# Performance work log

Hardware: AMD Instinct MI355X
Metric: run time of the kernel (lower is better)

Reference implementation:

```python
import jax, jax.numpy as jnp
import numpy as np

B, N, DIM, H, DH = 8, 1024, 768, 12, 64
INNER = H * DH
SCALE = DH ** -0.5


def _bias_idx(n):
    # Reproduce the offset->id mapping from the torch __init__ loop:
    # offsets are first seen in row-major (p1, p2) order, so
    # id(0)=0, id(-k)=k (k=1..n-1), id(+k)=n-1+k.
    i = np.arange(n)[:, None]
    j = np.arange(n)[None, :]
    off = i - j
    idx = np.where(off <= 0, -off, n - 1 + off)
    return jnp.asarray(idx, dtype=jnp.int32)  # (n, n), values in [0, 2n-2]


def setup_inputs() -> dict:
    key = jax.random.key(0)
    ks = jax.random.split(key, 5)
    x = jax.random.normal(ks[0], (B, N, DIM), dtype=jnp.float32)
    w_qkv = jax.random.normal(ks[1], (DIM, 3 * INNER), dtype=jnp.float32) * (DIM ** -0.5)
    bias_table = jax.random.normal(ks[2], (H, 2 * N - 1), dtype=jnp.float32) * 0.02
    w_out = jax.random.normal(ks[3], (INNER, DIM), dtype=jnp.float32) * (INNER ** -0.5)
    b_out = jnp.zeros((DIM,), dtype=jnp.float32)
    bias_idx = _bias_idx(N)
    return {"x": x, "w_qkv": w_qkv, "bias_table": bias_table,
            "w_out": w_out, "b_out": b_out, "bias_idx": bias_idx}


def reference(x, w_qkv, bias_table, w_out, b_out, bias_idx):
    b, n, _ = x.shape
    qkv = x @ w_qkv  # (b, n, 3*inner)
    q, k, v = jnp.split(qkv, 3, axis=-1)
    def heads(t):
        return t.reshape(b, n, H, DH).transpose(0, 2, 1, 3)  # (b, h, n, d)
    q, k, v = heads(q), heads(k), heads(v)
    bias = bias_table[:, bias_idx]  # (h, n, n), gathered per-head relpos bias
    dots = jnp.einsum('bhid,bhjd->bhij', q, k) * SCALE + bias[None]
    attn = jax.nn.softmax(dots, axis=-1)
    out = jnp.einsum('bhij,bhjd->bhid', attn, v)
    out = out.transpose(0, 2, 1, 3).reshape(b, n, INNER)
    return out @ w_out + b_out
```

## Files before the change

### kernel.cpp

```cpp
#include <hip/hip_runtime.h>
#include <hip/hip_bf16.h>
#include <stdint.h>

typedef unsigned short u16;
typedef unsigned int u32;
typedef __bf16 bf16x8 __attribute__((ext_vector_type(8)));
typedef float f32x4 __attribute__((ext_vector_type(4)));
typedef unsigned short u16x4 __attribute__((ext_vector_type(4)));
typedef unsigned int u32x2 __attribute__((ext_vector_type(2)));

#define SEQ     1024
#define DIM     768
#define NH      12
#define QKV_LD  2304
#define LOG2E   1.4426950408889634f
#define C1      0.18033688f

__device__ __forceinline__ u16 f2bf(float f) {
    union { float f; unsigned v; } x; x.f = f;
    unsigned r = (x.v + 0x7FFFu + ((x.v >> 16) & 1u)) >> 16;
    return (u16)r;
}
__device__ __forceinline__ void store_out(u16* p, float v)  { *p = f2bf(v); }
__device__ __forceinline__ void store_out(float* p, float v){ *p = v; }

__device__ __forceinline__ void async16(void* lds, const void* g) {
    __builtin_amdgcn_global_load_lds(
        (const __attribute__((address_space(1))) unsigned*)(uintptr_t)g,
        (__attribute__((address_space(3))) unsigned*)(unsigned)(uintptr_t)lds,
        16, 0, 0);
}

__device__ __forceinline__ int sw32(int row, int q) {
    return row * 32 + (q ^ ((row >> 1) & 3)) * 8;
}
__device__ __forceinline__ const bf16x8 ld64(const u16* base, int row, int cg) {
    return *(const bf16x8*)&base[row * 64 + (cg ^ (row & 7)) * 8];
}

__global__ __launch_bounds__(256) void cvt_k(const float* __restrict__ in,
                                             u16* __restrict__ out) {
    int i = (blockIdx.x * 256 + threadIdx.x) * 4;
    float4 v = *(const float4*)(in + i);
    u16x4 o = { f2bf(v.x), f2bf(v.y), f2bf(v.z), f2bf(v.w) };
    *(u16x4*)(out + i) = o;
}

__global__ __launch_bounds__(256) void transpose_k(const float* __restrict__ in,
                                                   u16* __restrict__ out,
                                                   int R, int C) {
    __shared__ __align__(16) float t[32][33];
    int c0 = blockIdx.x * 32, r0 = blockIdx.y * 32;
    int tx = threadIdx.x & 31, ty = threadIdx.x >> 5;
#pragma unroll
    for (int i = 0; i < 32; i += 8)
        t[ty + i][tx] = in[(size_t)(r0 + ty + i) * C + c0 + tx];
    __syncthreads();
#pragma unroll
    for (int i = 0; i < 32; i += 8)
        out[(size_t)(c0 + ty + i) * R + r0 + tx] = f2bf(t[tx][ty + i]);
}

__global__ __launch_bounds__(256) void vt_k(const u16* __restrict__ qkv,
                                            u16* __restrict__ vT) {
    __shared__ __align__(16) u16 t[32][33];
    int bh = blockIdx.z;
    int b = bh / 12, h = bh % 12;
    int key0 = blockIdx.x * 32, dh0 = blockIdx.y * 32;
    int tx = threadIdx.x & 31, ty = threadIdx.x >> 5;
#pragma unroll
    for (int i = 0; i < 32; i += 8)
        t[ty + i][tx] = qkv[(size_t)(b * SEQ + key0 + ty + i) * QKV_LD +
                            1536 + h * 64 + dh0 + tx];
    __syncthreads();
#pragma unroll
    for (int i = 0; i < 32; i += 8)
        vT[(size_t)(bh * 64 + dh0 + ty + i) * SEQ + key0 + tx] = t[tx][ty + i];
}

template <int HAS_BIAS, typename OUT_T>
__global__ __launch_bounds__(256) void gemm_bt(const u16* __restrict__ A,
                                               const u16* __restrict__ Bt,
                                               const float* __restrict__ bias,
                                               OUT_T* __restrict__ C,
                                               int M, int N, int K) {
    __shared__ __align__(16) u16 sA[128 * 32];
    __shared__ __align__(16) u16 sB[128 * 32];
    const int tid = threadIdx.x;
    const int lane = tid & 63;
    const int quad = lane >> 4, l16 = lane & 15;
    const int wave = tid >> 6;
    const int m0 = blockIdx.y * 128, n0 = blockIdx.x * 128;
    const int wm = (wave >> 1) * 64, wn = (wave & 1) * 64;

    f32x4 acc[4][4] = {};

    for (int k0 = 0; k0 < K; k0 += 32) {
        __syncthreads();
#pragma unroll
        for (int rep = 0; rep < 2; ++rep) {
            int i = rep * 256 + wave * 64 + lane;
            int row = i >> 2;
            int q = (i & 3) ^ ((row >> 1) & 3);
            async16(&sA[i * 8], A + (size_t)(m0 + row) * K + k0 + q * 8);
            async16(&sB[i * 8], Bt + (size_t)(n0 + row) * K + k0 + q * 8);
        }
        __syncthreads();

        bf16x8 af[4], bfr[4];
#pragma unroll
        for (int mi = 0; mi < 4; ++mi)
            af[mi] = *(const bf16x8*)&sA[sw32(wm + mi * 16 + l16, quad)];
#pragma unroll
        for (int nj = 0; nj < 4; ++nj)
            bfr[nj] = *(const bf16x8*)&sB[sw32(wn + nj * 16 + l16, quad)];
#pragma unroll
        for (int mi = 0; mi < 4; ++mi)
#pragma unroll
            for (int nj = 0; nj < 4; ++nj)
                acc[mi][nj] = __builtin_amdgcn_mfma_f32_16x16x32_bf16(
                    af[mi], bfr[nj], acc[mi][nj], 0, 0, 0);
    }

#pragma unroll
    for (int mi = 0; mi < 4; ++mi) {
#pragma unroll
        for (int nj = 0; nj < 4; ++nj) {
            int col = n0 + wn + nj * 16 + l16;
            float bv = HAS_BIAS ? bias[col] : 0.0f;
#pragma unroll
            for (int r = 0; r < 4; ++r) {
                int row = m0 + wm + mi * 16 + quad * 4 + r;
                store_out(&C[(size_t)row * N + col], acc[mi][nj][r] + bv);
            }
        }
    }
}

__global__ __launch_bounds__(256) void attn_k(const u16* __restrict__ qkv,
                                              const u16* __restrict__ vT,
                                              const float* __restrict__ bias_table,
                                              u16* __restrict__ out) {
    __shared__ __align__(16) u16 sK[64 * 64];
    __shared__ __align__(16) u16 sV[64 * 64];
    __shared__ __align__(16) float sBias[2048];
    __shared__ __align__(16) u16 sP[4][32 * 64];
    __shared__ __align__(16) float sLsum[4][32];

    const int tid = threadIdx.x;
    const int wave = tid >> 6, lane = tid & 63;
    const int quad = lane >> 4, l16 = lane & 15;
    const int h = blockIdx.y, b = blockIdx.z;
    const int q0 = blockIdx.x * 128, wq = wave * 32;

    for (int i = tid; i < 2047; i += 256)
        sBias[i] = LOG2E * bias_table[h * 2047 + (i <= 1023 ? 1023 - i : i)];

    bf16x8 qf[2][2];
#pragma unroll
    for (int nt = 0; nt < 2; ++nt)
#pragma unroll
        for (int hf = 0; hf < 2; ++hf)
            qf[nt][hf] = *(const bf16x8*)(qkv +
                (size_t)(b * SEQ + q0 + wq + nt * 16 + l16) * QKV_LD +
                h * 64 + hf * 32 + quad * 8);

    f32x4 o[2][4] = {};
    float lsum[2] = {0.f, 0.f};
    u16* sPw = sP[wave];

    for (int kt = 0; kt < SEQ / 64; ++kt) {
        __syncthreads();
#pragma unroll
        for (int rep = 0; rep < 2; ++rep) {
            int i = rep * 256 + wave * 64 + lane;
            int row = i >> 3;
            int c = (i & 7) ^ (row & 7);
            async16(&sK[i * 8],
                    qkv + (size_t)(b * SEQ + kt * 64 + row) * QKV_LD + 768 + h * 64 + c * 8);
            async16(&sV[i * 8],
                    vT + (size_t)((b * NH + h) * 64 + row) * SEQ + kt * 64 + c * 8);
        }
        __syncthreads();

#pragma unroll
        for (int mt = 0; mt < 4; ++mt) {
            int krow = mt * 16 + l16;
            bf16x8 af0 = ld64(sK, krow, quad);
            bf16x8 af1 = ld64(sK, krow, 4 + quad);
#pragma unroll
            for (int nt = 0; nt < 2; ++nt) {
                f32x4 s = {0.f, 0.f, 0.f, 0.f};
                s = __builtin_amdgcn_mfma_f32_16x16x32_bf16(af0, qf[nt][0], s, 0, 0, 0);
                s = __builtin_amdgcn_mfma_f32_16x16x32_bf16(af1, qf[nt][1], s, 0, 0, 0);
                int dbase = (q0 + wq + nt * 16 + l16) -
                            (kt * 64 + mt * 16 + quad * 4) + 1023;
                u32 u[4];
#pragma unroll
                for (int r = 0; r < 4; ++r) {
                    float arg = s[r] * C1 + sBias[dbase - r];
                    float p = exp2f(fminf(arg, 30.0f));
                    lsum[nt] += p;
                    u[r] = __float_as_uint(p) + 0x8000u;
                }
                u32x2 pk = { __builtin_amdgcn_perm(u[1], u[0], 0x07060302u),
                             __builtin_amdgcn_perm(u[3], u[2], 0x07060302u) };
                int qrow = nt * 16 + l16;
                int sc = (mt * 2 + (quad >> 1)) ^ (qrow & 7);
                *(u32x2*)&sPw[qrow * 64 + sc * 8 + (quad & 1) * 4] = pk;
            }
        }

        bf16x8 pf[2][2];
#pragma unroll
        for (int mtp = 0; mtp < 2; ++mtp) {
            int prow = mtp * 16 + l16;
            pf[mtp][0] = ld64(sPw, prow, quad);
            pf[mtp][1] = ld64(sPw, prow, 4 + quad);
        }
#pragma unroll
        for (int c4 = 0; c4 < 4; ++c4) {
            int vrow = c4 * 16 + l16;
            bf16x8 vf0 = ld64(sV, vrow, quad);
            bf16x8 vf1 = ld64(sV, vrow, 4 + quad);
#pragma unroll
            for (int mtp = 0; mtp < 2; ++mtp) {
                o[mtp][c4] = __builtin_amdgcn_mfma_f32_16x16x32_bf16(
                    pf[mtp][0], vf0, o[mtp][c4], 0, 0, 0);
                o[mtp][c4] = __builtin_amdgcn_mfma_f32_16x16x32_bf16(
                    pf[mtp][1], vf1, o[mtp][c4], 0, 0, 0);
            }
        }
    }

#pragma unroll
    for (int nt = 0; nt < 2; ++nt) {
        float s = lsum[nt];
        s += __shfl_xor(s, 16, 64);
        s += __shfl_xor(s, 32, 64);
        if (quad == 0) sLsum[wave][nt * 16 + l16] = s;
    }
#pragma unroll
    for (int mtp = 0; mtp < 2; ++mtp) {
        f32x4 ls = *(const f32x4*)&sLsum[wave][mtp * 16 + quad * 4];
#pragma unroll
        for (int c4 = 0; c4 < 4; ++c4)
#pragma unroll
            for (int r = 0; r < 4; ++r) {
                int qrow = q0 + wq + mtp * 16 + quad * 4 + r;
                out[(size_t)(b * SEQ + qrow) * DIM + h * 64 + c4 * 16 + l16] =
                    f2bf(o[mtp][c4][r] / ls[r]);
            }
    }
}

extern "C" void kernel_launch(void* const* d_in, const int* in_sizes, int n_in,
                              void* d_out, int out_size, void* d_ws, size_t ws_size,
                              hipStream_t stream) {
    const float* x          = (const float*)d_in[0];
    const float* w_qkv      = (const float*)d_in[1];
    const float* bias_table = (const float*)d_in[2];
    const float* w_out      = (const float*)d_in[3];
    const float* b_out      = (const float*)d_in[4];
    float* out = (float*)d_out;

    char* ws = (char*)d_ws;
    u16* ws_qkv   = (u16*)(ws);
    u16* ws_attn  = (u16*)(ws + 37748736);
    u16* ws_xb    = (u16*)(ws + 50331648);
    u16* ws_wqkvT = (u16*)(ws + 62914560);
    u16* ws_woutT = (u16*)(ws + 66453504);
    u16* ws_vT    = (u16*)(ws + 67633152);

    cvt_k<<<8 * 1024 * 768 / 1024, 256, 0, stream>>>(x, ws_xb);
    transpose_k<<<dim3(2304 / 32, 768 / 32), 256, 0, stream>>>(w_qkv, ws_wqkvT, 768, 2304);
    transpose_k<<<dim3(768 / 32, 768 / 32), 256, 0, stream>>>(w_out, ws_woutT, 768, 768);

    gemm_bt<0, u16><<<dim3(2304 / 128, 8192 / 128), 256, 0, stream>>>(
        ws_xb, ws_wqkvT, nullptr, ws_qkv, 8192, 2304, 768);

    vt_k<<<dim3(SEQ / 32, 2, 8 * NH), 256, 0, stream>>>(ws_qkv, ws_vT);

    attn_k<<<dim3(SEQ / 128, NH, 8), 256, 0, stream>>>(ws_qkv, ws_vT, bias_table, ws_attn);

    gemm_bt<1, float><<<dim3(768 / 128, 8192 / 128), 256, 0, stream>>>(
        ws_attn, ws_woutT, b_out, out, 8192, 768, 768);
}
```

Before: 230.6 us.

## Load K/V fragments directly from global memory and switch PV matmul to fp16

The attention kernel no longer stages K and V tiles in shared memory through async loads and two block-wide barriers per key tile. Each wave now reads its MFMA fragments straight from global memory and relies on the cache. V is stored transposed in fp16, P is packed to fp16 with cvt_pkrtz, and the PV product uses the f16 MFMA. The exp clamp is lowered to 15 so values stay within fp16 range. This drops the barriers and LDS traffic but makes each wave fetch the same K/V data separately, with uncoalesced strided global loads that may add latency.

New measurement: 263.1 us. 14.1% more time.

```diff
diff --git a/kernel.cpp b/kernel.cpp
--- a/kernel.cpp
+++ b/kernel.cpp
@@ -5,9 +5,11 @@
 typedef unsigned short u16;
 typedef unsigned int u32;
 typedef __bf16 bf16x8 __attribute__((ext_vector_type(8)));
+typedef _Float16 f16x8 __attribute__((ext_vector_type(8)));
+typedef _Float16 f16x2 __attribute__((ext_vector_type(2)));
+typedef __fp16 hf16x2 __attribute__((ext_vector_type(2)));
 typedef float f32x4 __attribute__((ext_vector_type(4)));
 typedef unsigned short u16x4 __attribute__((ext_vector_type(4)));
-typedef unsigned int u32x2 __attribute__((ext_vector_type(2)));
 
 #define SEQ     1024
 #define DIM     768
@@ -16,6 +18,9 @@
 #define LOG2E   1.4426950408889634f
 #define C1      0.18033688f
 
+__device__ __forceinline__ float bf2f(u16 u) {
+    union { unsigned v; float f; } x; x.v = ((unsigned)u) << 16; return x.f;
+}
 __device__ __forceinline__ u16 f2bf(float f) {
     union { float f; unsigned v; } x; x.f = f;
     unsigned r = (x.v + 0x7FFFu + ((x.v >> 16) & 1u)) >> 16;
@@ -33,9 +38,6 @@
 
 __device__ __forceinline__ int sw32(int row, int q) {
     return row * 32 + (q ^ ((row >> 1) & 3)) * 8;
-}
-__device__ __forceinline__ const bf16x8 ld64(const u16* base, int row, int cg) {
-    return *(const bf16x8*)&base[row * 64 + (cg ^ (row & 7)) * 8];
 }
 
 __global__ __launch_bounds__(256) void cvt_k(const float* __restrict__ in,
@@ -62,7 +64,7 @@
 }
 
 __global__ __launch_bounds__(256) void vt_k(const u16* __restrict__ qkv,
-                                            u16* __restrict__ vT) {
+                                            _Float16* __restrict__ vT) {
     __shared__ __align__(16) u16 t[32][33];
     int bh = blockIdx.z;
     int b = bh / 12, h = bh % 12;
@@ -75,7 +77,8 @@
     __syncthreads();
 #pragma unroll
     for (int i = 0; i < 32; i += 8)
-        vT[(size_t)(bh * 64 + dh0 + ty + i) * SEQ + key0 + tx] = t[tx][ty + i];
+        vT[(size_t)(bh * 64 + dh0 + ty + i) * SEQ + key0 + tx] =
+            (_Float16)bf2f(t[tx][ty + i]);
 }
 
 template <int HAS_BIAS, typename OUT_T>
@@ -138,13 +141,11 @@
 }
 
 __global__ __launch_bounds__(256) void attn_k(const u16* __restrict__ qkv,
-                                              const u16* __restrict__ vT,
+                                              const _Float16* __restrict__ vT,
                                               const float* __restrict__ bias_table,
                                               u16* __restrict__ out) {
-    __shared__ __align__(16) u16 sK[64 * 64];
-    __shared__ __align__(16) u16 sV[64 * 64];
+    __shared__ __align__(16) _Float16 sP[4][32 * 64];
     __shared__ __align__(16) float sBias[2048];
-    __shared__ __align__(16) u16 sP[4][32 * 64];
     __shared__ __align__(16) float sLsum[4][32];
 
     const int tid = threadIdx.x;
@@ -165,29 +166,21 @@
                 (size_t)(b * SEQ + q0 + wq + nt * 16 + l16) * QKV_LD +
                 h * 64 + hf * 32 + quad * 8);
 
+    __syncthreads();
+
+    const u16* kbase = qkv + (size_t)b * SEQ * QKV_LD + 768 + h * 64 + quad * 8;
+    const _Float16* vbase = vT + (size_t)(b * NH + h) * 64 * SEQ + quad * 8;
+
     f32x4 o[2][4] = {};
     float lsum[2] = {0.f, 0.f};
-    u16* sPw = sP[wave];
+    _Float16* sPw = sP[wave];
 
     for (int kt = 0; kt < SEQ / 64; ++kt) {
-        __syncthreads();
-#pragma unroll
-        for (int rep = 0; rep < 2; ++rep) {
-            int i = rep * 256 + wave * 64 + lane;
-            int row = i >> 3;
-            int c = (i & 7) ^ (row & 7);
-            async16(&sK[i * 8],
-                    qkv + (size_t)(b * SEQ + kt * 64 + row) * QKV_LD + 768 + h * 64 + c * 8);
-            async16(&sV[i * 8],
-                    vT + (size_t)((b * NH + h) * 64 + row) * SEQ + kt * 64 + c * 8);
-        }
-        __syncthreads();
-
 #pragma unroll
         for (int mt = 0; mt < 4; ++mt) {
-            int krow = mt * 16 + l16;
-            bf16x8 af0 = ld64(sK, krow, quad);
-            bf16x8 af1 = ld64(sK, krow, 4 + quad);
+            int krow = kt * 64 + mt * 16 + l16;
+            bf16x8 af0 = *(const bf16x8*)(kbase + (size_t)krow * QKV_LD);
+            bf16x8 af1 = *(const bf16x8*)(kbase + (size_t)krow * QKV_LD + 32);
 #pragma unroll
             for (int nt = 0; nt < 2; ++nt) {
                 f32x4 s = {0.f, 0.f, 0.f, 0.f};
@@ -195,39 +188,43 @@
                 s = __builtin_amdgcn_mfma_f32_16x16x32_bf16(af1, qf[nt][1], s, 0, 0, 0);
                 int dbase = (q0 + wq + nt * 16 + l16) -
                             (kt * 64 + mt * 16 + quad * 4) + 1023;
-                u32 u[4];
+                float p[4];
 #pragma unroll
                 for (int r = 0; r < 4; ++r) {
                     float arg = s[r] * C1 + sBias[dbase - r];
-                    float p = exp2f(fminf(arg, 30.0f));
-                    lsum[nt] += p;
-                    u[r] = __float_as_uint(p) + 0x8000u;
+                    p[r] = exp2f(fminf(arg, 15.0f));
+                    lsum[nt] += p[r];
                 }
-                u32x2 pk = { __builtin_amdgcn_perm(u[1], u[0], 0x07060302u),
-                             __builtin_amdgcn_perm(u[3], u[2], 0x07060302u) };
+                f16x2 pk0 = __builtin_bit_cast(f16x2, __builtin_amdgcn_cvt_pkrtz(p[0], p[1]));
+                f16x2 pk1 = __builtin_bit_cast(f16x2, __builtin_amdgcn_cvt_pkrtz(p[2], p[3]));
                 int qrow = nt * 16 + l16;
-                int sc = (mt * 2 + (quad >> 1)) ^ (qrow & 7);
-                *(u32x2*)&sPw[qrow * 64 + sc * 8 + (quad & 1) * 4] = pk;
-            }
-        }
-
-        bf16x8 pf[2][2];
+                int slot = (mt * 2 + (quad >> 1)) ^ (qrow & 7);
+                _Float16* dst = &sPw[qrow * 64 + slot * 8 + (quad & 1) * 4];
+                *(f16x2*)dst       = pk0;
+                *(f16x2*)(dst + 2) = pk1;
+            }
+        }
+
+        f16x8 pf[2][2];
 #pragma unroll
         for (int mtp = 0; mtp < 2; ++mtp) {
             int prow = mtp * 16 + l16;
-            pf[mtp][0] = ld64(sPw, prow, quad);
-            pf[mtp][1] = ld64(sPw, prow, 4 + quad);
+#pragma unroll
+            for (int hf = 0; hf < 2; ++hf) {
+                int slot = (hf * 4 + quad) ^ (prow & 7);
+                pf[mtp][hf] = *(const f16x8*)&sPw[prow * 64 + slot * 8];
+            }
         }
 #pragma unroll
         for (int c4 = 0; c4 < 4; ++c4) {
-            int vrow = c4 * 16 + l16;
-            bf16x8 vf0 = ld64(sV, vrow, quad);
-            bf16x8 vf1 = ld64(sV, vrow, 4 + quad);
+            const _Float16* vrow = vbase + (size_t)(c4 * 16 + l16) * SEQ + kt * 64;
+            f16x8 vf0 = *(const f16x8*)vrow;
+            f16x8 vf1 = *(const f16x8*)(vrow + 32);
 #pragma unroll
             for (int mtp = 0; mtp < 2; ++mtp) {
-                o[mtp][c4] = __builtin_amdgcn_mfma_f32_16x16x32_bf16(
+                o[mtp][c4] = __builtin_amdgcn_mfma_f32_16x16x32_f16(
                     pf[mtp][0], vf0, o[mtp][c4], 0, 0, 0);
-                o[mtp][c4] = __builtin_amdgcn_mfma_f32_16x16x32_bf16(
+                o[mtp][c4] = __builtin_amdgcn_mfma_f32_16x16x32_f16(
                     pf[mtp][1], vf1, o[mtp][c4], 0, 0, 0);
             }
         }
@@ -265,12 +262,12 @@
     float* out = (float*)d_out;
 
     char* ws = (char*)d_ws;
-    u16* ws_qkv   = (u16*)(ws);
-    u16* ws_attn  = (u16*)(ws + 37748736);
-    u16* ws_xb    = (u16*)(ws + 50331648);
-    u16* ws_wqkvT = (u16*)(ws + 62914560);
-    u16* ws_woutT = (u16*)(ws + 66453504);
-    u16* ws_vT    = (u16*)(ws + 67633152);
+    u16* ws_qkv        = (u16*)(ws);
+    u16* ws_attn       = (u16*)(ws + 37748736);
+    u16* ws_xb         = (u16*)(ws + 50331648);
+    u16* ws_wqkvT      = (u16*)(ws + 62914560);
+    u16* ws_woutT      = (u16*)(ws + 66453504);
+    _Float16* ws_vT    = (_Float16*)(ws + 67633152);
 
     cvt_k<<<8 * 1024 * 768 / 1024, 256, 0, stream>>>(x, ws_xb);
     transpose_k<<<dim3(2304 / 32, 768 / 32), 256, 0, stream>>>(w_qkv, ws_wqkvT, 768, 2304);
```
